# Performance work log

Measured on AMD Instinct MI355X. Metric: run time of the kernel, lower is better.

The kernel has to match this reference:

```python
import jax, jax.numpy as jnp
import numpy as np

N = 100000
E = 6400000
IN_CH = 128
HID = 5
H1 = 2
OUT = 10
H2 = 1
EPS_BN = 1e-5


def glorot(key, shape):
    fan = shape[0] + shape[-1]
    s = jnp.sqrt(6.0 / fan)
    return jax.random.uniform(key, shape, jnp.float32, -s, s)


def setup_inputs() -> dict:
    key = jax.random.key(0)
    ks = jax.random.split(key, 12)
    x = jax.random.normal(ks[0], (N, IN_CH), jnp.float32)
    edge_index = jax.random.randint(ks[1], (2, E), 0, N, jnp.int64)
    return {
        "x": x,
        "W1": glorot(ks[2], (IN_CH, H1 * HID)),
        "a_src1": glorot(ks[3], (H1, HID)),
        "a_dst1": glorot(ks[4], (H1, HID)),
        "b1": jnp.zeros((H1 * HID,), jnp.float32),
        "gamma1": jnp.ones((H1 * HID,), jnp.float32),
        "beta1": jnp.zeros((H1 * HID,), jnp.float32),
        "W2": glorot(ks[5], (H1 * HID, H2 * OUT)),
        "a_src2": glorot(ks[6], (H2, OUT)),
        "a_dst2": glorot(ks[7], (H2, OUT)),
        "b2": jnp.zeros((OUT,), jnp.float32),
        "edge_index": edge_index,
    }


def gat_conv(x, src, dst, W, a_src, a_dst, bias, heads, out_ch, concat):
    n = x.shape[0]
    h = (x @ W).reshape(n, heads, out_ch)          # [N,H,C]
    alpha_s = (h * a_src).sum(-1)                  # [N,H]
    alpha_d = (h * a_dst).sum(-1)                  # [N,H]
    e = jax.nn.leaky_relu(alpha_s[src] + alpha_d[dst], 0.2)  # [E,H]
    emax = jax.ops.segment_max(e, dst, num_segments=n)
    emax = jnp.where(jnp.isfinite(emax), emax, 0.0)
    ex = jnp.exp(e - jax.lax.stop_gradient(emax)[dst])
    denom = jax.ops.segment_sum(ex, dst, num_segments=n)
    alpha = ex / (denom[dst] + 1e-16)              # edge softmax by target
    msg = h[src] * alpha[..., None]                # [E,H,C]
    out = jax.ops.segment_sum(msg, dst, num_segments=n)
    out = out.reshape(n, heads * out_ch) if concat else out.mean(axis=1)
    return out + bias


def batch_norm(x, gamma, beta):
    mu = x.mean(0)
    var = ((x - mu) ** 2).mean(0)
    return (x - mu) * jax.lax.rsqrt(var + EPS_BN) * gamma + beta


def reference(x, W1, a_src1, a_dst1, b1, gamma1, beta1, W2, a_src2, a_dst2, b2, edge_index):
    n = x.shape[0]
    loop = jnp.arange(n, dtype=edge_index.dtype)   # add_self_loops=True
    src = jnp.concatenate([edge_index[0], loop])
    dst = jnp.concatenate([edge_index[1], loop])
    h = gat_conv(x, src, dst, W1, a_src1, a_dst1, b1, H1, HID, True)
    h = batch_norm(h, gamma1, beta1)
    h = jax.nn.elu(h)
    out = gat_conv(h, src, dst, W2, a_src2, a_dst2, b2, H2, OUT, False)
    return out
```

## Files before the change

kernel.cpp:

```cpp
#include <hip/hip_runtime.h>
#include <hip/hip_fp16.h>
#include <math.h>

#define NN 100000
#define NE 6400000
#define INCH 128
#define BSH 7
#define BW (1 << BSH)
#define NBKT ((NN + BW - 1) / BW)
#define NBP 784
#define BCAP 9216
#define BIN_CH 8192
#define BNP 800

__device__ inline float pkh(float a, float b) {
  __half2 h = __floats2half2_rn(a, b);
  return __uint_as_float(*reinterpret_cast<unsigned int*>(&h));
}
__device__ inline float2 uph(float f) {
  unsigned int b = __float_as_uint(f);
  __half2 h = *reinterpret_cast<__half2*>(&b);
  return __half22float2(h);
}

__global__ __launch_bounds__(256) void k_count(const int* __restrict__ ei,
                                               int* __restrict__ cntmat) {
  __shared__ int cnt4[4][NBKT];
  int t = threadIdx.x;
  int w = t >> 6;
  for (int i = t; i < 4 * NBKT; i += 256) (&cnt4[0][0])[i] = 0;
  __syncthreads();
  int c0 = blockIdx.x * BIN_CH;
  int c1 = c0 + BIN_CH < NE ? c0 + BIN_CH : NE;
  for (int i = c0 + t; i < c1; i += 256)
    atomicAdd(&cnt4[w][ei[NE + i] >> BSH], 1);
  __syncthreads();
  for (int b = t; b < NBKT; b += 256)
    cntmat[(size_t)b * NBP + blockIdx.x] =
        cnt4[0][b] + cnt4[1][b] + cnt4[2][b] + cnt4[3][b];
}

__global__ __launch_bounds__(64) void k_scanb(const int* __restrict__ cntmat,
                                              int* __restrict__ basemat,
                                              int* __restrict__ bcnt) {
  int j = blockIdx.x;
  int lane = threadIdx.x;
  int carry = 0;
  for (int i0 = 0; i0 < NBKT; i0 += 64) {
    int i = i0 + lane;
    int v0 = (i < NBKT) ? cntmat[(size_t)j * NBP + i] : 0;
    int v = v0;
#pragma unroll
    for (int off = 1; off < 64; off <<= 1) {
      int u = __shfl_up(v, off, 64);
      if (lane >= off) v += u;
    }
    if (i < NBKT) basemat[(size_t)i * NBP + j] = carry + v - v0;
    carry += __shfl(v, 63, 64);
  }
  if (lane == 0) bcnt[j] = carry;
}

__global__ __launch_bounds__(256) void k_scatter2(
    const int* __restrict__ ei, const int* __restrict__ cntmat,
    const int* __restrict__ basemat, unsigned int* __restrict__ pairs) {
  __shared__ int offs[NBKT];
  __shared__ int cur[NBKT];
  __shared__ int gbase[NBKT];
  __shared__ int scanp[256];
  __shared__ unsigned int stage[BIN_CH];
  __shared__ unsigned short sbkt[BIN_CH];
  int t = threadIdx.x;
  int chunk = blockIdx.x;
  int myb0 = t * 4;
  int tots[4];
  int asum = 0;
#pragma unroll
  for (int j = 0; j < 4; j++) {
    int b = myb0 + j;
    int tt = (b < NBKT) ? cntmat[(size_t)b * NBP + chunk] : 0;
    tots[j] = tt;
    asum += tt;
  }
  for (int b = t; b < NBKT; b += 256)
    gbase[b] = basemat[(size_t)chunk * NBP + b];
  scanp[t] = asum;
  __syncthreads();
  for (int off = 1; off < 256; off <<= 1) {
    int v = (t >= off) ? scanp[t - off] : 0;
    __syncthreads();
    scanp[t] += v;
    __syncthreads();
  }
  int run = (t == 0) ? 0 : scanp[t - 1];
#pragma unroll
  for (int j = 0; j < 4; j++) {
    int b = myb0 + j;
    if (b < NBKT) {
      offs[b] = run;
      cur[b] = run;
      run += tots[j];
    }
  }
  __syncthreads();
  int c0 = chunk * BIN_CH;
  int c1 = c0 + BIN_CH < NE ? c0 + BIN_CH : NE;
  for (int i = c0 + t; i < c1; i += 256) {
    int s = ei[i], d = ei[NE + i];
    int bkt = d >> BSH;
    int pos = atomicAdd(&cur[bkt], 1);
    stage[pos] = ((unsigned int)s << BSH) | (unsigned int)(d & (BW - 1));
    sbkt[pos] = (unsigned short)bkt;
  }
  __syncthreads();
  int total = c1 - c0;
  for (int i = t; i < total; i += 256) {
    unsigned int e = stage[i];
    int b = sbkt[i];
    int gp = gbase[b] + (i - offs[b]);
    if (gp < BCAP) pairs[(size_t)b * BCAP + gp] = e;
  }
}

__global__ __launch_bounds__(256) void k_l1_node(
    const float* __restrict__ x, const float* __restrict__ W1,
    const float* __restrict__ a_src1, const float* __restrict__ a_dst1,
    float* __restrict__ h1, float2* __restrict__ ad1) {
  __shared__ float Wt[10 * INCH];
  __shared__ float asw[10], adw[10];
  for (int i = threadIdx.x; i < 10 * INCH; i += blockDim.x) {
    int c = i / 10, k = i - c * 10;
    Wt[k * INCH + c] = W1[i];
  }
  if (threadIdx.x < 10) {
    asw[threadIdx.x] = a_src1[threadIdx.x];
    adw[threadIdx.x] = a_dst1[threadIdx.x];
  }
  __syncthreads();
  int n = blockIdx.x * blockDim.x + threadIdx.x;
  if (n >= NN) return;
  const float4* xr = (const float4*)(x + (size_t)n * INCH);
  const float4* Wt4 = (const float4*)Wt;
  float acc[10];
#pragma unroll
  for (int k = 0; k < 10; k++) acc[k] = 0.f;
#pragma unroll 8
  for (int c4 = 0; c4 < INCH / 4; c4++) {
    float4 xv = xr[c4];
#pragma unroll
    for (int k = 0; k < 10; k++) {
      float4 wv = Wt4[k * (INCH / 4) + c4];
      acc[k] += xv.x * wv.x + xv.y * wv.y + xv.z * wv.z + xv.w * wv.w;
    }
  }
  float s0 = 0.f, s1 = 0.f, d0 = 0.f, d1 = 0.f;
#pragma unroll
  for (int j = 0; j < 5; j++) {
    s0 += acc[j] * asw[j];
    s1 += acc[5 + j] * asw[5 + j];
    d0 += acc[j] * adw[j];
    d1 += acc[5 + j] * adw[5 + j];
  }
  float4* hrow = (float4*)(h1 + (size_t)n * 8);
  hrow[0] = make_float4(pkh(acc[0], acc[1]), pkh(acc[2], acc[3]),
                        pkh(acc[4], acc[5]), pkh(acc[6], acc[7]));
  hrow[1] = make_float4(pkh(acc[8], acc[9]), 0.f, s0, s1);
  ad1[n] = make_float2(d0, d1);
}

__global__ __launch_bounds__(512, 6) void k_l1_aggs(
    const int* __restrict__ bcnt, const unsigned int* __restrict__ pairs,
    const float* __restrict__ h1, const float2* __restrict__ ad1,
    const float* __restrict__ b1, float* __restrict__ g1,
    float* __restrict__ bn_part) {
  __shared__ int cnt8[8][BW];
  __shared__ int wb[8][BW];
  __shared__ int offs[BW];
  __shared__ int tot[BW];
  __shared__ int scanbuf[BW];
  __shared__ unsigned int sorted[BCAP];
  __shared__ float biasS[10];
  __shared__ float bn_lds[8 * 20];
  int t = threadIdx.x;
  int w = t >> 6;
  int b = blockIdx.x;
  int base_n = b << BSH;
  int nloc = NN - base_n < BW ? NN - base_n : BW;
  for (int i = t; i < 8 * BW; i += 512) (&cnt8[0][0])[i] = 0;
  if (t < 10) biasS[t] = b1[t];
  __syncthreads();
  int cntb = bcnt[b];
  cntb = cntb > BCAP ? BCAP : cntb;
  const unsigned int* pp = pairs + (size_t)b * BCAP;
  for (int k = t; k < cntb; k += 512)
    atomicAdd(&cnt8[w][pp[k] & (BW - 1)], 1);
  __syncthreads();
  if (t < BW) {
    int tt = 0;
#pragma unroll
    for (int j = 0; j < 8; j++) tt += cnt8[j][t];
    tot[t] = tt;
    scanbuf[t] = tt;
  }
  __syncthreads();
  for (int step = 1; step < BW; step <<= 1) {
    int v = 0;
    if (t < BW && t >= step) v = scanbuf[t - step];
    __syncthreads();
    if (t < BW) scanbuf[t] += v;
    __syncthreads();
  }
  if (t < BW) {
    int run = scanbuf[t] - tot[t];
    offs[t] = run;
#pragma unroll
    for (int j = 0; j < 8; j++) { wb[j][t] = run; run += cnt8[j][t]; cnt8[j][t] = 0; }
  }
  __syncthreads();
  for (int k = t; k < cntb; k += 512) {
    unsigned int e = pp[k];
    int dl = e & (BW - 1);
    int pos = wb[w][dl] + atomicAdd(&cnt8[w][dl], 1);
    sorted[pos] = e >> BSH;
  }
  __syncthreads();
  int node = t >> 2;
  int part = t & 3;
  bool valid = node < nloc;
  int n = base_n + node;
  float acc[10];
#pragma unroll
  for (int j = 0; j < 10; j++) acc[j] = 0.f;
  float den0 = 0.f, den1 = 0.f;
  float2 adn = valid ? ad1[n] : make_float2(0.f, 0.f);
  int s0i = offs[node], c = valid ? tot[node] : 0;
  for (int k = part; k < c; k += 4) {
    int s = (int)sorted[s0i + k];
    const float4* hs = (const float4*)(h1 + (size_t)s * 8);
    float4 ra = hs[0], rb = hs[1];
    float e0 = rb.z + adn.x; e0 = e0 > 0.f ? e0 : 0.2f * e0;
    float e1 = rb.w + adn.y; e1 = e1 > 0.f ? e1 : 0.2f * e1;
    float x0 = expf(e0), x1 = expf(e1);
    float2 h01 = uph(ra.x), h23 = uph(ra.y), h45 = uph(ra.z), h67 = uph(ra.w),
           h89 = uph(rb.x);
    acc[0] += x0 * h01.x;  acc[1] += x0 * h01.y;  acc[2] += x0 * h23.x;
    acc[3] += x0 * h23.y;  acc[4] += x0 * h45.x;
    acc[5] += x1 * h45.y;  acc[6] += x1 * h67.x;  acc[7] += x1 * h67.y;
    acc[8] += x1 * h89.x;  acc[9] += x1 * h89.y;
    den0 += x0; den1 += x1;
  }
#pragma unroll
  for (int j = 0; j < 10; j++) {
    acc[j] += __shfl_xor(acc[j], 1, 64);
    acc[j] += __shfl_xor(acc[j], 2, 64);
  }
  den0 += __shfl_xor(den0, 1, 64); den0 += __shfl_xor(den0, 2, 64);
  den1 += __shfl_xor(den1, 1, 64); den1 += __shfl_xor(den1, 2, 64);
  float v[10];
#pragma unroll
  for (int j = 0; j < 10; j++) v[j] = 0.f;
  if (part == 0 && valid) {
    const float4* hs = (const float4*)(h1 + (size_t)n * 8);
    float4 ra = hs[0], rb = hs[1];
    float e0 = rb.z + adn.x; e0 = e0 > 0.f ? e0 : 0.2f * e0;
    float e1 = rb.w + adn.y; e1 = e1 > 0.f ? e1 : 0.2f * e1;
    float x0 = expf(e0), x1 = expf(e1);
    float2 h01 = uph(ra.x), h23 = uph(ra.y), h45 = uph(ra.z), h67 = uph(ra.w),
           h89 = uph(rb.x);
    acc[0] += x0 * h01.x;  acc[1] += x0 * h01.y;  acc[2] += x0 * h23.x;
    acc[3] += x0 * h23.y;  acc[4] += x0 * h45.x;
    acc[5] += x1 * h45.y;  acc[6] += x1 * h67.x;  acc[7] += x1 * h67.y;
    acc[8] += x1 * h89.x;  acc[9] += x1 * h89.y;
    den0 += x0; den1 += x1;
    float i0 = 1.f / (den0 + 1e-16f), i1 = 1.f / (den1 + 1e-16f);
#pragma unroll
    for (int j = 0; j < 5; j++) v[j] = acc[j] * i0 + biasS[j];
#pragma unroll
    for (int j = 5; j < 10; j++) v[j] = acc[j] * i1 + biasS[j];
    float4* gr = (float4*)(g1 + (size_t)n * 12);
    gr[0] = make_float4(v[0], v[1], v[2], v[3]);
    gr[1] = make_float4(v[4], v[5], v[6], v[7]);
    gr[2] = make_float4(v[8], v[9], 0.f, 0.f);
  }
  float s[20];
#pragma unroll
  for (int j = 0; j < 10; j++) { s[j] = v[j]; s[10 + j] = v[j] * v[j]; }
#pragma unroll
  for (int j = 0; j < 20; j++) {
    for (int off = 32; off > 0; off >>= 1) s[j] += __shfl_down(s[j], off, 64);
  }
  if ((t & 63) == 0) {
#pragma unroll
    for (int j = 0; j < 20; j++) bn_lds[w * 20 + j] = s[j];
  }
  __syncthreads();
  if (t == 0) {
#pragma unroll
    for (int j = 0; j < 20; j++) {
      float acc20 = 0.f;
#pragma unroll
      for (int ww = 0; ww < 8; ww++) acc20 += bn_lds[ww * 20 + j];
      bn_part[j * BNP + b] = acc20;
    }
  }
}

__global__ __launch_bounds__(64) void k_bnred(const float* __restrict__ bn_part,
                                              float* __restrict__ bns) {
  int j = blockIdx.x;
  int lane = threadIdx.x;
  float s = 0.f;
  for (int b = lane; b < NBKT; b += 64) s += bn_part[j * BNP + b];
#pragma unroll
  for (int off = 32; off > 0; off >>= 1) s += __shfl_down(s, off, 64);
  if (lane == 0) bns[j] = s;
}

__global__ __launch_bounds__(256) void k_l2_node(
    const float* __restrict__ g1, const float* __restrict__ bns,
    const float* __restrict__ gamma1, const float* __restrict__ beta1,
    const float* __restrict__ W2, const float* __restrict__ a_src2,
    const float* __restrict__ a_dst2, float* __restrict__ h2,
    float* __restrict__ ad2) {
  __shared__ float scale[10], shift[10], W2s[100], a2s[10], a2d[10];
  if (threadIdx.x < 10) {
    int j = threadIdx.x;
    float mu = bns[j] * (1.f / NN);
    float var = bns[10 + j] * (1.f / NN) - mu * mu;
    float rs = rsqrtf(var + 1e-5f);
    scale[j] = rs * gamma1[j];
    shift[j] = beta1[j] - mu * rs * gamma1[j];
    a2s[j] = a_src2[j];
    a2d[j] = a_dst2[j];
  }
  for (int i = threadIdx.x; i < 100; i += blockDim.x) W2s[i] = W2[i];
  __syncthreads();
  int n = blockIdx.x * blockDim.x + threadIdx.x;
  if (n >= NN) return;
  const float4* gr = (const float4*)(g1 + (size_t)n * 12);
  float4 g0 = gr[0], g1v = gr[1], g2 = gr[2];
  float hv[10] = {g0.x, g0.y, g0.z, g0.w, g1v.x, g1v.y, g1v.z, g1v.w, g2.x, g2.y};
#pragma unroll
  for (int j = 0; j < 10; j++) {
    float t = hv[j] * scale[j] + shift[j];
    hv[j] = t > 0.f ? t : expm1f(t);
  }
  float o[10];
#pragma unroll
  for (int k = 0; k < 10; k++) o[k] = 0.f;
#pragma unroll
  for (int c = 0; c < 10; c++) {
#pragma unroll
    for (int k = 0; k < 10; k++) o[k] += hv[c] * W2s[c * 10 + k];
  }
  float ss = 0.f, sd = 0.f;
#pragma unroll
  for (int k = 0; k < 10; k++) { ss += o[k] * a2s[k]; sd += o[k] * a2d[k]; }
  float4* hr = (float4*)(h2 + (size_t)n * 8);
  hr[0] = make_float4(pkh(o[0], o[1]), pkh(o[2], o[3]), pkh(o[4], o[5]),
                      pkh(o[6], o[7]));
  hr[1] = make_float4(pkh(o[8], o[9]), 0.f, ss, 0.f);
  ad2[n] = sd;
}

__global__ __launch_bounds__(512, 6) void k_l2_aggs(
    const int* __restrict__ bcnt, const unsigned int* __restrict__ pairs,
    const float* __restrict__ h2, const float* __restrict__ ad2,
    const float* __restrict__ b2, float* __restrict__ out) {
  __shared__ int cnt8[8][BW];
  __shared__ int wb[8][BW];
  __shared__ int offs[BW];
  __shared__ int tot[BW];
  __shared__ int scanbuf[BW];
  __shared__ unsigned int sorted[BCAP];
  __shared__ float biasS[10];
  int t = threadIdx.x;
  int w = t >> 6;
  int b = blockIdx.x;
  int base_n = b << BSH;
  int nloc = NN - base_n < BW ? NN - base_n : BW;
  for (int i = t; i < 8 * BW; i += 512) (&cnt8[0][0])[i] = 0;
  if (t < 10) biasS[t] = b2[t];
  __syncthreads();
  int cntb = bcnt[b];
  cntb = cntb > BCAP ? BCAP : cntb;
  const unsigned int* pp = pairs + (size_t)b * BCAP;
  for (int k = t; k < cntb; k += 512)
    atomicAdd(&cnt8[w][pp[k] & (BW - 1)], 1);
  __syncthreads();
  if (t < BW) {
    int tt = 0;
#pragma unroll
    for (int j = 0; j < 8; j++) tt += cnt8[j][t];
    tot[t] = tt;
    scanbuf[t] = tt;
  }
  __syncthreads();
  for (int step = 1; step < BW; step <<= 1) {
    int v = 0;
    if (t < BW && t >= step) v = scanbuf[t - step];
    __syncthreads();
    if (t < BW) scanbuf[t] += v;
    __syncthreads();
  }
  if (t < BW) {
    int run = scanbuf[t] - tot[t];
    offs[t] = run;
#pragma unroll
    for (int j = 0; j < 8; j++) { wb[j][t] = run; run += cnt8[j][t]; cnt8[j][t] = 0; }
  }
  __syncthreads();
  for (int k = t; k < cntb; k += 512) {
    unsigned int e = pp[k];
    int dl = e & (BW - 1);
    int pos = wb[w][dl] + atomicAdd(&cnt8[w][dl], 1);
    sorted[pos] = e >> BSH;
  }
  __syncthreads();
  int node = t >> 2;
  int part = t & 3;
  bool valid = node < nloc;
  int n = base_n + node;
  float acc[10];
#pragma unroll
  for (int j = 0; j < 10; j++) acc[j] = 0.f;
  float den = 0.f;
  float adn = valid ? ad2[n] : 0.f;
  int s0i = offs[node], c = valid ? tot[node] : 0;
  for (int k = part; k < c; k += 4) {
    int s = (int)sorted[s0i + k];
    const float4* hs = (const float4*)(h2 + (size_t)s * 8);
    float4 ra = hs[0], rb = hs[1];
    float ee = rb.z + adn; ee = ee > 0.f ? ee : 0.2f * ee;
    float xv = expf(ee);
    float2 h01 = uph(ra.x), h23 = uph(ra.y), h45 = uph(ra.z), h67 = uph(ra.w),
           h89 = uph(rb.x);
    acc[0] += xv * h01.x;  acc[1] += xv * h01.y;  acc[2] += xv * h23.x;
    acc[3] += xv * h23.y;  acc[4] += xv * h45.x;  acc[5] += xv * h45.y;
    acc[6] += xv * h67.x;  acc[7] += xv * h67.y;  acc[8] += xv * h89.x;
    acc[9] += xv * h89.y;
    den += xv;
  }
#pragma unroll
  for (int j = 0; j < 10; j++) {
    acc[j] += __shfl_xor(acc[j], 1, 64);
    acc[j] += __shfl_xor(acc[j], 2, 64);
  }
  den += __shfl_xor(den, 1, 64); den += __shfl_xor(den, 2, 64);
  if (part == 0 && valid) {
    const float4* hs = (const float4*)(h2 + (size_t)n * 8);
    float4 ra = hs[0], rb = hs[1];
    float ee = rb.z + adn; ee = ee > 0.f ? ee : 0.2f * ee;
    float xv = expf(ee);
    float2 h01 = uph(ra.x), h23 = uph(ra.y), h45 = uph(ra.z), h67 = uph(ra.w),
           h89 = uph(rb.x);
    acc[0] += xv * h01.x;  acc[1] += xv * h01.y;  acc[2] += xv * h23.x;
    acc[3] += xv * h23.y;  acc[4] += xv * h45.x;  acc[5] += xv * h45.y;
    acc[6] += xv * h67.x;  acc[7] += xv * h67.y;  acc[8] += xv * h89.x;
    acc[9] += xv * h89.y;
    den += xv;
    float inv = 1.f / (den + 1e-16f);
    float2* orow = (float2*)(out + (size_t)n * 10);
    orow[0] = make_float2(acc[0] * inv + biasS[0], acc[1] * inv + biasS[1]);
    orow[1] = make_float2(acc[2] * inv + biasS[2], acc[3] * inv + biasS[3]);
    orow[2] = make_float2(acc[4] * inv + biasS[4], acc[5] * inv + biasS[5]);
    orow[3] = make_float2(acc[6] * inv + biasS[6], acc[7] * inv + biasS[7]);
    orow[4] = make_float2(acc[8] * inv + biasS[8], acc[9] * inv + biasS[9]);
  }
}

extern "C" void kernel_launch(void* const* d_in, const int* in_sizes, int n_in,
                              void* d_out, int out_size, void* d_ws, size_t ws_size,
                              hipStream_t stream) {
  const float* x      = (const float*)d_in[0];
  const float* W1     = (const float*)d_in[1];
  const float* a_src1 = (const float*)d_in[2];
  const float* a_dst1 = (const float*)d_in[3];
  const float* b1     = (const float*)d_in[4];
  const float* gamma1 = (const float*)d_in[5];
  const float* beta1  = (const float*)d_in[6];
  const float* W2     = (const float*)d_in[7];
  const float* a_src2 = (const float*)d_in[8];
  const float* a_dst2 = (const float*)d_in[9];
  const float* b2     = (const float*)d_in[10];
  const int*   ei     = (const int*)d_in[11];
  float* out = (float*)d_out;

  int* bcnt = (int*)d_ws;
  unsigned int* pairs = (unsigned int*)d_ws + 1024;
  float* h1 = (float*)(pairs + (size_t)NBKT * BCAP);
  float* ad1 = h1 + (size_t)NN * 8;
  float* g1 = ad1 + (size_t)NN * 2;
  float* h2 = g1 + (size_t)NN * 12;
  float* ad2 = h2 + (size_t)NN * 8;
  float* bn_part = ad2 + NN;
  float* bns = bn_part + 20 * BNP;
  int* cntmat = (int*)(bns + 20 + 12);
  int* basemat = cntmat + (size_t)NBKT * NBP;

  const int B = 256;
  const int gN = (NN + B - 1) / B;
  const int gBin = (NE + BIN_CH - 1) / BIN_CH;

  k_count<<<gBin, B, 0, stream>>>(ei, cntmat);
  k_scanb<<<NBKT, 64, 0, stream>>>(cntmat, basemat, bcnt);
  k_scatter2<<<gBin, B, 0, stream>>>(ei, cntmat, basemat, pairs);
  k_l1_node<<<gN, B, 0, stream>>>(x, W1, a_src1, a_dst1, h1, (float2*)ad1);
  k_l1_aggs<<<NBKT, 512, 0, stream>>>(bcnt, pairs, h1, (const float2*)ad1, b1,
                                      g1, bn_part);
  k_bnred<<<20, 64, 0, stream>>>(bn_part, bns);
  k_l2_node<<<gN, B, 0, stream>>>(g1, bns, gamma1, beta1, W2, a_src2, a_dst2,
                                  h2, ad2);
  k_l2_aggs<<<NBKT, 512, 0, stream>>>(bcnt, pairs, h2, ad2, b2, out);
}
```

Baseline: 361.7 us.

## Sort bucket edges once in a separate kernel and reuse in both aggregations

```diff
diff --git a/kernel.cpp b/kernel.cpp
--- a/kernel.cpp
+++ b/kernel.cpp
@@ -122,6 +122,59 @@
   }
 }
 
+__global__ __launch_bounds__(512, 6) void k_sortb(
+    const int* __restrict__ bcnt, unsigned int* __restrict__ pairs,
+    unsigned int* __restrict__ oc) {
+  __shared__ int cnt8[8][BW];
+  __shared__ int wb[8][BW];
+  __shared__ int tot[BW];
+  __shared__ int scanbuf[BW];
+  __shared__ unsigned int sorted[BCAP];
+  int t = threadIdx.x;
+  int w = t >> 6;
+  int b = blockIdx.x;
+  int base_n = b << BSH;
+  for (int i = t; i < 8 * BW; i += 512) (&cnt8[0][0])[i] = 0;
+  __syncthreads();
+  int cntb = bcnt[b];
+  cntb = cntb > BCAP ? BCAP : cntb;
+  unsigned int* pp = pairs + (size_t)b * BCAP;
+  for (int k = t; k < cntb; k += 512)
+    atomicAdd(&cnt8[w][pp[k] & (BW - 1)], 1);
+  __syncthreads();
+  if (t < BW) {
+    int tt = 0;
+#pragma unroll
+    for (int j = 0; j < 8; j++) tt += cnt8[j][t];
+    tot[t] = tt;
+    scanbuf[t] = tt;
+  }
+  __syncthreads();
+  for (int step = 1; step < BW; step <<= 1) {
+    int v = 0;
+    if (t < BW && t >= step) v = scanbuf[t - step];
+    __syncthreads();
+    if (t < BW) scanbuf[t] += v;
+    __syncthreads();
+  }
+  if (t < BW) {
+    int run = scanbuf[t] - tot[t];
+    int n = base_n + t;
+    if (n < NN) oc[n] = ((unsigned int)run << 16) | (unsigned int)tot[t];
+#pragma unroll
+    for (int j = 0; j < 8; j++) { wb[j][t] = run; run += cnt8[j][t]; cnt8[j][t] = 0; }
+  }
+  __syncthreads();
+  for (int k = t; k < cntb; k += 512) {
+    unsigned int e = pp[k];
+    int dl = e & (BW - 1);
+    int pos = wb[w][dl] + atomicAdd(&cnt8[w][dl], 1);
+    sorted[pos] = e >> BSH;
+  }
+  __syncthreads();
+  for (int k = t; k < cntb; k += 512) pp[k] = sorted[k];
+}
+
 __global__ __launch_bounds__(256) void k_l1_node(
     const float* __restrict__ x, const float* __restrict__ W1,
     const float* __restrict__ a_src1, const float* __restrict__ a_dst1,
@@ -168,74 +221,35 @@
   ad1[n] = make_float2(d0, d1);
 }
 
-__global__ __launch_bounds__(512, 6) void k_l1_aggs(
-    const int* __restrict__ bcnt, const unsigned int* __restrict__ pairs,
+__global__ __launch_bounds__(512, 8) void k_l1_aggs(
+    const unsigned int* __restrict__ sorted_g, const unsigned int* __restrict__ oc,
     const float* __restrict__ h1, const float2* __restrict__ ad1,
     const float* __restrict__ b1, float* __restrict__ g1,
     float* __restrict__ bn_part) {
-  __shared__ int cnt8[8][BW];
-  __shared__ int wb[8][BW];
-  __shared__ int offs[BW];
-  __shared__ int tot[BW];
-  __shared__ int scanbuf[BW];
-  __shared__ unsigned int sorted[BCAP];
   __shared__ float biasS[10];
   __shared__ float bn_lds[8 * 20];
   int t = threadIdx.x;
   int w = t >> 6;
   int b = blockIdx.x;
   int base_n = b << BSH;
-  int nloc = NN - base_n < BW ? NN - base_n : BW;
-  for (int i = t; i < 8 * BW; i += 512) (&cnt8[0][0])[i] = 0;
   if (t < 10) biasS[t] = b1[t];
-  __syncthreads();
-  int cntb = bcnt[b];
-  cntb = cntb > BCAP ? BCAP : cntb;
-  const unsigned int* pp = pairs + (size_t)b * BCAP;
-  for (int k = t; k < cntb; k += 512)
-    atomicAdd(&cnt8[w][pp[k] & (BW - 1)], 1);
-  __syncthreads();
-  if (t < BW) {
-    int tt = 0;
-#pragma unroll
-    for (int j = 0; j < 8; j++) tt += cnt8[j][t];
-    tot[t] = tt;
-    scanbuf[t] = tt;
-  }
-  __syncthreads();
-  for (int step = 1; step < BW; step <<= 1) {
-    int v = 0;
-    if (t < BW && t >= step) v = scanbuf[t - step];
-    __syncthreads();
-    if (t < BW) scanbuf[t] += v;
-    __syncthreads();
-  }
-  if (t < BW) {
-    int run = scanbuf[t] - tot[t];
-    offs[t] = run;
-#pragma unroll
-    for (int j = 0; j < 8; j++) { wb[j][t] = run; run += cnt8[j][t]; cnt8[j][t] = 0; }
-  }
-  __syncthreads();
-  for (int k = t; k < cntb; k += 512) {
-    unsigned int e = pp[k];
-    int dl = e & (BW - 1);
-    int pos = wb[w][dl] + atomicAdd(&cnt8[w][dl], 1);
-    sorted[pos] = e >> BSH;
-  }
   __syncthreads();
   int node = t >> 2;
   int part = t & 3;
-  bool valid = node < nloc;
   int n = base_n + node;
+  bool valid = n < NN;
+  unsigned int ocv = valid ? oc[n] : 0u;
+  int s0i = (int)(ocv >> 16);
+  int c = (int)(ocv & 0xffffu);
+  float2 adn = valid ? ad1[n] : make_float2(0.f, 0.f);
+  const unsigned int* sp = sorted_g + (size_t)b * BCAP + s0i;
   float acc[10];
 #pragma unroll
   for (int j = 0; j < 10; j++) acc[j] = 0.f;
   float den0 = 0.f, den1 = 0.f;
-  float2 adn = valid ? ad1[n] : make_float2(0.f, 0.f);
-  int s0i = offs[node], c = valid ? tot[node] : 0;
+#pragma unroll 2
   for (int k = part; k < c; k += 4) {
-    int s = (int)sorted[s0i + k];
+    int s = (int)sp[k];
     const float4* hs = (const float4*)(h1 + (size_t)s * 8);
     float4 ra = hs[0], rb = hs[1];
     float e0 = rb.z + adn.x; e0 = e0 > 0.f ? e0 : 0.2f * e0;
@@ -287,7 +301,10 @@
   for (int j = 0; j < 10; j++) { s[j] = v[j]; s[10 + j] = v[j] * v[j]; }
 #pragma unroll
   for (int j = 0; j < 20; j++) {
-    for (int off = 32; off > 0; off >>= 1) s[j] += __shfl_down(s[j], off, 64);
+    s[j] += __shfl_down(s[j], 4, 64);
+    s[j] += __shfl_down(s[j], 8, 64);
+    s[j] += __shfl_down(s[j], 16, 64);
+    s[j] += __shfl_down(s[j], 32, 64);
   }
   if ((t & 63) == 0) {
 #pragma unroll
@@ -363,72 +380,32 @@
   ad2[n] = sd;
 }
 
-__global__ __launch_bounds__(512, 6) void k_l2_aggs(
-    const int* __restrict__ bcnt, const unsigned int* __restrict__ pairs,
+__global__ __launch_bounds__(512, 8) void k_l2_aggs(
+    const unsigned int* __restrict__ sorted_g, const unsigned int* __restrict__ oc,
     const float* __restrict__ h2, const float* __restrict__ ad2,
     const float* __restrict__ b2, float* __restrict__ out) {
-  __shared__ int cnt8[8][BW];
-  __shared__ int wb[8][BW];
-  __shared__ int offs[BW];
-  __shared__ int tot[BW];
-  __shared__ int scanbuf[BW];
-  __shared__ unsigned int sorted[BCAP];
   __shared__ float biasS[10];
   int t = threadIdx.x;
-  int w = t >> 6;
   int b = blockIdx.x;
   int base_n = b << BSH;
-  int nloc = NN - base_n < BW ? NN - base_n : BW;
-  for (int i = t; i < 8 * BW; i += 512) (&cnt8[0][0])[i] = 0;
   if (t < 10) biasS[t] = b2[t];
-  __syncthreads();
-  int cntb = bcnt[b];
-  cntb = cntb > BCAP ? BCAP : cntb;
-  const unsigned int* pp = pairs + (size_t)b * BCAP;
-  for (int k = t; k < cntb; k += 512)
-    atomicAdd(&cnt8[w][pp[k] & (BW - 1)], 1);
-  __syncthreads();
-  if (t < BW) {
-    int tt = 0;
-#pragma unroll
-    for (int j = 0; j < 8; j++) tt += cnt8[j][t];
-    tot[t] = tt;
-    scanbuf[t] = tt;
-  }
-  __syncthreads();
-  for (int step = 1; step < BW; step <<= 1) {
-    int v = 0;
-    if (t < BW && t >= step) v = scanbuf[t - step];
-    __syncthreads();
-    if (t < BW) scanbuf[t] += v;
-    __syncthreads();
-  }
-  if (t < BW) {
-    int run = scanbuf[t] - tot[t];
-    offs[t] = run;
-#pragma unroll
-    for (int j = 0; j < 8; j++) { wb[j][t] = run; run += cnt8[j][t]; cnt8[j][t] = 0; }
-  }
-  __syncthreads();
-  for (int k = t; k < cntb; k += 512) {
-    unsigned int e = pp[k];
-    int dl = e & (BW - 1);
-    int pos = wb[w][dl] + atomicAdd(&cnt8[w][dl], 1);
-    sorted[pos] = e >> BSH;
-  }
   __syncthreads();
   int node = t >> 2;
   int part = t & 3;
-  bool valid = node < nloc;
   int n = base_n + node;
+  bool valid = n < NN;
+  unsigned int ocv = valid ? oc[n] : 0u;
+  int s0i = (int)(ocv >> 16);
+  int c = (int)(ocv & 0xffffu);
+  float adn = valid ? ad2[n] : 0.f;
+  const unsigned int* sp = sorted_g + (size_t)b * BCAP + s0i;
   float acc[10];
 #pragma unroll
   for (int j = 0; j < 10; j++) acc[j] = 0.f;
   float den = 0.f;
-  float adn = valid ? ad2[n] : 0.f;
-  int s0i = offs[node], c = valid ? tot[node] : 0;
+#pragma unroll 2
   for (int k = part; k < c; k += 4) {
-    int s = (int)sorted[s0i + k];
+    int s = (int)sp[k];
     const float4* hs = (const float4*)(h2 + (size_t)s * 8);
     float4 ra = hs[0], rb = hs[1];
     float ee = rb.z + adn; ee = ee > 0.f ? ee : 0.2f * ee;
@@ -497,6 +474,7 @@
   float* bns = bn_part + 20 * BNP;
   int* cntmat = (int*)(bns + 20 + 12);
   int* basemat = cntmat + (size_t)NBKT * NBP;
+  unsigned int* oc = (unsigned int*)(basemat + (size_t)NBKT * NBP);
 
   const int B = 256;
   const int gN = (NN + B - 1) / B;
@@ -505,11 +483,12 @@
   k_count<<<gBin, B, 0, stream>>>(ei, cntmat);
   k_scanb<<<NBKT, 64, 0, stream>>>(cntmat, basemat, bcnt);
   k_scatter2<<<gBin, B, 0, stream>>>(ei, cntmat, basemat, pairs);
+  k_sortb<<<NBKT, 512, 0, stream>>>(bcnt, pairs, oc);
   k_l1_node<<<gN, B, 0, stream>>>(x, W1, a_src1, a_dst1, h1, (float2*)ad1);
-  k_l1_aggs<<<NBKT, 512, 0, stream>>>(bcnt, pairs, h1, (const float2*)ad1, b1,
+  k_l1_aggs<<<NBKT, 512, 0, stream>>>(pairs, oc, h1, (const float2*)ad1, b1,
                                       g1, bn_part);
   k_bnred<<<20, 64, 0, stream>>>(bn_part, bns);
   k_l2_node<<<gN, B, 0, stream>>>(g1, bns, gamma1, beta1, W2, a_src2, a_dst2,
                                   h2, ad2);
-  k_l2_aggs<<<NBKT, 512, 0, stream>>>(bcnt, pairs, h2, ad2, b2, out);
-}
+  k_l2_aggs<<<NBKT, 512, 0, stream>>>(pairs, oc, h2, ad2, b2, out);
+}
```

Result: slower. 399.7 us (+10.5%).
